# Kernel optimization log

Hardware: AMD Instinct MI355X
Metric: run time of the kernel (lower is better)

## Reference

```python
import jax, jax.numpy as jnp
import numpy as np
from jax import lax

NUM_CLASSES = 80
TOPK = 13
ALPHA = 1.0
BETA = 6.0
EPS = 1e-9
P = 150000
N = 256


def _make_boxes(key, n, scale):
    k1, k2 = jax.random.split(key)
    xy = jax.random.uniform(k1, (n, 2), dtype=jnp.float32) * scale
    wh = jax.random.uniform(k2, (n, 2), dtype=jnp.float32) * (0.2 * scale) + 1.0
    return jnp.concatenate([xy, xy + wh], axis=-1)  # valid x1y1x2y2


def setup_inputs() -> dict:
    key = jax.random.key(0)
    k1, k2, k3, k4 = jax.random.split(key, 4)
    cls_pred = jax.random.uniform(k1, (P, NUM_CLASSES), dtype=jnp.float32)
    bbox_pred = _make_boxes(k2, P, 640.0)
    bbox_gt = _make_boxes(k3, N, 640.0)
    # FG labels are > 0 (code indexes cls_pred[label-1])
    label_gt = jax.random.randint(k4, (N, 1), 1, NUM_CLASSES + 1, dtype=jnp.int32)
    return {"cls_pred": cls_pred, "bbox_pred": bbox_pred, "label_gt": label_gt, "bbox_gt": bbox_gt}


def _ious(bbox1, bbox2, eps=EPS):
    # bbox1: (N,4) gt, bbox2: (P,4) pred -> (N,P)
    b1 = bbox1[:, None, :]
    b2 = bbox2[None, :, :]
    x1y1 = jnp.maximum(b1[..., 0:2], b2[..., 0:2])
    x2y2 = jnp.minimum(b1[..., 2:4], b2[..., 2:4])
    inter = jnp.clip(x2y2 - x1y1, 0.0).prod(-1)
    area1 = jnp.clip(b1[..., 2:4] - b1[..., 0:2], 0.0).prod(-1)
    area2 = jnp.clip(b2[..., 2:4] - b2[..., 0:2], 0.0).prod(-1)
    return inter / (area1 + area2 - inter + eps)


def _metrics_topk(metrics, topk, eps=EPS):
    n, num_priors = metrics.shape
    topk_vals, topk_idxs = lax.top_k(metrics, topk)  # (N,k)
    keep = topk_vals.max(axis=-1, keepdims=True) > eps
    topk_idxs = jnp.where(keep, topk_idxs, 0)
    rows = jnp.arange(n)[:, None]
    counts = jnp.zeros((n, num_priors), jnp.int32).at[rows, topk_idxs].add(1)
    is_in_topk = jnp.where(counts > 1, 0, counts)
    return is_in_topk.astype(metrics.dtype)


def reference(cls_pred, bbox_pred, label_gt, bbox_gt):
    num_priors, num_classes = cls_pred.shape
    n_gt = bbox_gt.shape[0]
    ious = _ious(bbox_gt, bbox_pred)  # (N,P)
    lbl = label_gt.reshape(-1).astype(jnp.int32)  # (N,)
    bbox_cls_scores = jnp.take(cls_pred.T, lbl - 1, axis=0)  # (N,P)
    alignment_metrics = jnp.power(bbox_cls_scores, ALPHA) * jnp.power(ious, BETA)
    mask_positive = _metrics_topk(alignment_metrics, TOPK)  # (N,P) float 0/1
    mask_positive_sum = mask_positive.sum(axis=0)  # (P,)
    # conflict resolution: priors claimed by >1 gt go to the max-iou gt.
    # Applying unconditionally equals the torch data-dependent branch.
    is_max_iou = (jnp.arange(n_gt)[:, None] == ious.argmax(axis=0)[None, :]).astype(ious.dtype)
    mask_positive = jnp.where(mask_positive_sum[None, :] > 1, is_max_iou, mask_positive)
    mask_positive_sum = mask_positive.sum(axis=0)
    assigned_gt_index = mask_positive.argmax(axis=0)  # (P,)
    assigned_labels = lbl[assigned_gt_index]  # (P,)
    assigned_cls = jax.nn.one_hot(assigned_labels - 1, num_classes, dtype=jnp.int32)
    assigned_bboxes = bbox_gt[assigned_gt_index]  # (P,4)
    assigned_labels = jnp.where(mask_positive_sum > 0, assigned_labels, 0)
    return (assigned_gt_index, assigned_labels, assigned_cls, assigned_bboxes)
```

## Files before the change

### kernel.cpp

```cpp
#include <hip/hip_runtime.h>

#define TOPK 13
#define NCLS 80
#define EPSF 1e-9f
#define NSEG 32
#define GPB  8
#define CAP2 832

__global__ __launch_bounds__(256) void sortgt(const int* __restrict__ lbl,
                                              int* __restrict__ gorder, int N) {
    __shared__ int key[256];
    int t = threadIdx.x;
    key[t] = (t < N) ? ((lbl[t] << 8) | t) : 0x7FFFFFFF;
    __syncthreads();
    for (int k = 2; k <= 256; k <<= 1) {
        for (int j = k >> 1; j >= 1; j >>= 1) {
            int ixj = t ^ j;
            if (ixj > t) {
                int a = key[t], b = key[ixj];
                bool up = ((t & k) == 0);
                if (up ? (a > b) : (a < b)) { key[t] = b; key[ixj] = a; }
            }
            __syncthreads();
        }
    }
    if (t < N) gorder[t] = key[t] & 0xFF;
}

__global__ __launch_bounds__(256) void prep(const float4* __restrict__ cls4,
                                            float* __restrict__ clsT,
                                            int* __restrict__ count,
                                            int* __restrict__ firstg, int P) {
    __shared__ float tile[64 * 81];
    int p0 = blockIdx.x * 64;
    int valid = P - p0; if (valid > 64) valid = 64;
    int t = threadIdx.x;
    int limq = valid * 20;
    for (int f = t; f < 64 * 20; f += 256) {
        int pl = f / 20, cq = f - pl * 20;
        float4 v = (f < limq) ? cls4[(size_t)p0 * 20 + f] : make_float4(0, 0, 0, 0);
        tile[pl * 81 + 4 * cq + 0] = v.x;
        tile[pl * 81 + 4 * cq + 1] = v.y;
        tile[pl * 81 + 4 * cq + 2] = v.z;
        tile[pl * 81 + 4 * cq + 3] = v.w;
    }
    if (t < 64 && t < valid) { count[p0 + t] = 0; firstg[p0 + t] = 0x7FFFFFFF; }
    __syncthreads();
    for (int f = t; f < 80 * 16; f += 256) {
        int c = f >> 4, j4 = f & 15;
        int j = 4 * j4;
        if (j < valid) {
            float4 o;
            o.x = tile[(j + 0) * 81 + c];
            o.y = tile[(j + 1) * 81 + c];
            o.z = tile[(j + 2) * 81 + c];
            o.w = tile[(j + 3) * 81 + c];
            *(float4*)&clsT[(size_t)c * P + p0 + j] = o;
        }
    }
}

__global__ __launch_bounds__(512, 4) void phaseA1(const float* __restrict__ clsT,
                                                  const float4* __restrict__ bboxp,
                                                  const float4* __restrict__ bboxg,
                                                  const int* __restrict__ lbl,
                                                  const int* __restrict__ gorder,
                                                  float2* __restrict__ cand,
                                                  int P, int N, int seglen) {
#pragma clang fp contract(off)
    const int s = blockIdx.x, tile = blockIdx.y, t = threadIdx.x;
    const int wv = t >> 6, lane = t & 63;
    const int pstart = s * seglen;
    int pend = pstart + seglen; if (pend > P) pend = P;

    __shared__ float2 buf[GPB][CAP2];
    __shared__ int ctr[GPB];

    float4 gb[GPB]; float ga[GPB]; int coff[GPB];
#pragma unroll
    for (int j = 0; j < GPB; j++) {
        int gi8 = tile * GPB + j;
        int gj = (gi8 < N) ? gorder[gi8] : -1;
        if (gj >= 0) {
            gb[j] = bboxg[gj];
            int c = lbl[gj] - 1;
            coff[j] = c * P;
        } else {
            gb[j] = make_float4(0.0f, 0.0f, 0.0f, 0.0f);
            coff[j] = 0;
        }
        ga[j] = fmaxf(gb[j].z - gb[j].x, 0.0f) * fmaxf(gb[j].w - gb[j].y, 0.0f);
    }
    const bool myValid = (tile * GPB + wv) < N;
    if (t < GPB) ctr[t] = 0;
    __syncthreads();

    bool first = true;
    for (int p = pstart + t; p < pend; p += 512) {
        float4 pb = bboxp[p];
        float pa = fmaxf(pb.z - pb.x, 0.0f) * fmaxf(pb.w - pb.y, 0.0f);
        bool force = first && (t < 16);
        first = false;
        float sc[GPB];
#pragma unroll
        for (int j = 0; j < GPB; j++) sc[j] = clsT[coff[j] + p];
#pragma unroll
        for (int j = 0; j < GPB; j++) {
            float xx1 = fmaxf(gb[j].x, pb.x), yy1 = fmaxf(gb[j].y, pb.y);
            float xx2 = fminf(gb[j].z, pb.z), yy2 = fminf(gb[j].w, pb.w);
            float inter = fmaxf(xx2 - xx1, 0.0f) * fmaxf(yy2 - yy1, 0.0f);
            float iou = inter / (((ga[j] + pa) - inter) + EPSF);
            float i2 = iou * iou;
            float m = sc[j] * ((i2 * i2) * i2);
            bool want = (m > 0.0f) || force;
            if (want) {
                int slot = atomicAdd(&ctr[j], 1);
                if (slot < CAP2) buf[j][slot] = make_float2(m, __int_as_float(p));
            }
        }
    }
    __syncthreads();

    const int total = ctr[wv];
    float v[TOPK]; int id[TOPK];
#pragma unroll
    for (int k = 0; k < TOPK; k++) { v[k] = -1.0f; id[k] = 0x7FFFFFFF; }

    auto ins = [&](float m, int p) {
        bool b12 = (m > v[TOPK - 1]) || (m == v[TOPK - 1] && p < id[TOPK - 1]);
        if (b12) {
#pragma unroll
            for (int k = TOPK - 1; k >= 1; k--) {
                bool a = (m > v[k - 1]) || (m == v[k - 1] && p < id[k - 1]);
                bool b = (m > v[k]) || (m == v[k] && p < id[k]);
                float nv = a ? v[k - 1] : (b ? m : v[k]);
                int   ni = a ? id[k - 1] : (b ? p : id[k]);
                v[k] = nv; id[k] = ni;
            }
            bool a0 = (m > v[0]) || (m == v[0] && p < id[0]);
            if (a0) { v[0] = m; id[0] = p; }
        }
    };

    if (total <= CAP2) {
        for (int e = lane; e < total; e += 64) {
            float2 E = buf[wv][e];
            ins(E.x, __float_as_int(E.y));
        }
    } else if (myValid) {
        int gj = gorder[tile * GPB + wv];
        float4 gbw = bboxg[gj];
        float gaw = fmaxf(gbw.z - gbw.x, 0.0f) * fmaxf(gbw.w - gbw.y, 0.0f);
        const float* crow = clsT + (size_t)(lbl[gj] - 1) * P;
        for (int p = pstart + lane; p < pend; p += 64) {
            float4 pb = bboxp[p];
            float pa = fmaxf(pb.z - pb.x, 0.0f) * fmaxf(pb.w - pb.y, 0.0f);
            float xx1 = fmaxf(gbw.x, pb.x), yy1 = fmaxf(gbw.y, pb.y);
            float xx2 = fminf(gbw.z, pb.z), yy2 = fminf(gbw.w, pb.w);
            float inter = fmaxf(xx2 - xx1, 0.0f) * fmaxf(yy2 - yy1, 0.0f);
            float iou = inter / (((gaw + pa) - inter) + EPSF);
            float i2 = iou * iou;
            float m = crow[p] * ((i2 * i2) * i2);
            ins(m, p);
        }
    }
    __syncthreads();

    float2* wl = buf[wv];
#pragma unroll
    for (int k = 0; k < TOPK; k++)
        wl[lane * TOPK + k] = make_float2(v[k], __int_as_float(id[k]));
    __syncthreads();
    for (int str = 32; str >= 1; str >>= 1) {
        if (lane < str) {
            float2 merged[TOPK];
            int a = 0, b = 0;
            const int ba = lane * TOPK, bb = (lane + str) * TOPK;
#pragma unroll
            for (int k = 0; k < TOPK; k++) {
                float2 fa = wl[ba + a], fb = wl[bb + b];
                int ia = __float_as_int(fa.y), ib = __float_as_int(fb.y);
                bool takeA = (fa.x > fb.x) || (fa.x == fb.x && ia < ib);
                merged[k] = takeA ? fa : fb;
                a += takeA; b += !takeA;
            }
#pragma unroll
            for (int k = 0; k < TOPK; k++) wl[ba + k] = merged[k];
        }
        __syncthreads();
    }
    if (lane < TOPK && myValid) {
        int gj = gorder[tile * GPB + wv];
        cand[((size_t)gj * NSEG + s) * TOPK + lane] = wl[lane];
    }
}

__global__ __launch_bounds__(512) void phaseA2(const float2* __restrict__ cand,
                                               int* __restrict__ count,
                                               int* __restrict__ firstg) {
    const int g = blockIdx.x;
    const int t = threadIdx.x;
    const int M = NSEG * TOPK;
    __shared__ float cv[512];
    __shared__ int   ci[512];
    if (t < M) {
        float2 e = cand[(size_t)g * M + t];
        cv[t] = e.x; ci[t] = __float_as_int(e.y);
    } else {
        cv[t] = -1.0f; ci[t] = 0x7FFFFFFF;
    }
    __syncthreads();
    for (int k = 2; k <= 512; k <<= 1) {
        for (int j = k >> 1; j >= 1; j >>= 1) {
            int ixj = t ^ j;
            if (ixj > t) {
                float va = cv[t], vb = cv[ixj];
                int   ia = ci[t], ib = ci[ixj];
                bool aBeforeB = (va > vb) || (va == vb && ia < ib);
                bool dirFwd = ((t & k) == 0);
                bool doswap = dirFwd ? !aBeforeB : aBeforeB;
                if (doswap) { cv[t] = vb; ci[t] = ib; cv[ixj] = va; ci[ixj] = ia; }
            }
            __syncthreads();
        }
    }
    if (t < TOPK && cv[0] > EPSF) {
        int pi = ci[t];
        atomicAdd(&count[pi], 1);
        atomicMin(&firstg[pi], g);
    }
}

__global__ __launch_bounds__(256) void phaseCF(const float4* __restrict__ bboxp,
                                               const float4* __restrict__ bboxg,
                                               const int* __restrict__ lbl,
                                               const int* __restrict__ count,
                                               const int* __restrict__ firstg,
                                               float* __restrict__ out0,
                                               float* __restrict__ out1,
                                               float4* __restrict__ outcls4,
                                               float4* __restrict__ outbox4, int P, int N) {
#pragma clang fp contract(off)
    __shared__ float4 gbS[256];
    __shared__ int glS[256];
    __shared__ int gil[256];
    __shared__ int clsl[256];
    int t = threadIdx.x;
    if (t < N) { gbS[t] = bboxg[t]; glS[t] = lbl[t]; }
    __syncthreads();
    int p0 = blockIdx.x * 256;
    int nloc = P - p0; if (nloc > 256) nloc = 256;
    if (t < nloc) {
        int p = p0 + t;
        int cnt = count[p];
        int gi = 0, pos = 0;
        if (cnt == 1) { gi = firstg[p]; pos = 1; }
        else if (cnt > 1) {
            float4 pb = bboxp[p];
            float pa = fmaxf(pb.z - pb.x, 0.0f) * fmaxf(pb.w - pb.y, 0.0f);
            float best = -1.0f;
            for (int g = 0; g < N; g++) {
                float4 g4 = gbS[g];
                float gar = fmaxf(g4.z - g4.x, 0.0f) * fmaxf(g4.w - g4.y, 0.0f);
                float xx1 = fmaxf(g4.x, pb.x), yy1 = fmaxf(g4.y, pb.y);
                float xx2 = fminf(g4.z, pb.z), yy2 = fminf(g4.w, pb.w);
                float inter = fmaxf(xx2 - xx1, 0.0f) * fmaxf(yy2 - yy1, 0.0f);
                float iou = inter / (((gar + pa) - inter) + EPSF);
                if (iou > best) { best = iou; gi = g; }
            }
            pos = 1;
        }
        out0[p] = (float)gi;
        out1[p] = pos ? (float)glS[gi] : 0.0f;
        gil[t] = gi;
        clsl[t] = glS[gi] - 1;
        outbox4[p] = gbS[gi];
    }
    __syncthreads();
    for (int f = t; f < nloc * 20; f += 256) {
        int pl = f / 20, q = f - pl * 20;
        int cl = clsl[pl], c0 = q * 4;
        float4 vv = make_float4(c0 == cl ? 1.0f : 0.0f, c0 + 1 == cl ? 1.0f : 0.0f,
                                c0 + 2 == cl ? 1.0f : 0.0f, c0 + 3 == cl ? 1.0f : 0.0f);
        outcls4[(size_t)p0 * 20 + f] = vv;
    }
}

__global__ __launch_bounds__(256) void phaseC1(const float4* __restrict__ bboxp,
                                               const float4* __restrict__ bboxg,
                                               const int* __restrict__ lbl,
                                               const int* __restrict__ count,
                                               const int* __restrict__ firstg,
                                               float* __restrict__ out0,
                                               float* __restrict__ out1, int P, int N) {
#pragma clang fp contract(off)
    __shared__ float4 gbS[256];
    __shared__ int glS[256];
    if (threadIdx.x < (unsigned)N) {
        gbS[threadIdx.x] = bboxg[threadIdx.x];
        glS[threadIdx.x] = lbl[threadIdx.x];
    }
    __syncthreads();
    int p = blockIdx.x * 256 + threadIdx.x;
    if (p >= P) return;
    int cnt = count[p];
    int gi = 0, pos = 0;
    if (cnt == 1) { gi = firstg[p]; pos = 1; }
    else if (cnt > 1) {
        float4 pb = bboxp[p];
        float pa = fmaxf(pb.z - pb.x, 0.0f) * fmaxf(pb.w - pb.y, 0.0f);
        float best = -1.0f;
        for (int g = 0; g < N; g++) {
            float4 g4 = gbS[g];
            float gar = fmaxf(g4.z - g4.x, 0.0f) * fmaxf(g4.w - g4.y, 0.0f);
            float xx1 = fmaxf(g4.x, pb.x), yy1 = fmaxf(g4.y, pb.y);
            float xx2 = fminf(g4.z, pb.z), yy2 = fminf(g4.w, pb.w);
            float inter = fmaxf(xx2 - xx1, 0.0f) * fmaxf(yy2 - yy1, 0.0f);
            float iou = inter / (((gar + pa) - inter) + EPSF);
            if (iou > best) { best = iou; gi = g; }
        }
        pos = 1;
    }
    out0[p] = (float)gi;
    out1[p] = pos ? (float)glS[gi] : 0.0f;
}

__global__ __launch_bounds__(256) void phaseC2(const float4* __restrict__ bboxg,
                                               const int* __restrict__ lbl,
                                               const float* __restrict__ out0,
                                               float* __restrict__ outcls,
                                               float* __restrict__ outbox, int P, int N) {
    __shared__ float gbb[256 * 4];
    __shared__ int glS[256];
    __shared__ int clsl[256];
    __shared__ int gil[256];
    int tid = threadIdx.x;
    if (tid < N) {
        float4 b = bboxg[tid];
        gbb[tid * 4 + 0] = b.x; gbb[tid * 4 + 1] = b.y;
        gbb[tid * 4 + 2] = b.z; gbb[tid * 4 + 3] = b.w;
        glS[tid] = lbl[tid];
    }
    __syncthreads();
    int p0 = blockIdx.x * 256;
    int nloc = P - p0; if (nloc > 256) nloc = 256;
    if (tid < nloc) {
        int gi = (int)out0[p0 + tid];
        gil[tid] = gi;
        clsl[tid] = glS[gi] - 1;
    }
    __syncthreads();
    for (int f = tid; f < nloc * NCLS; f += 256) {
        int pl = f / NCLS;
        int c  = f - pl * NCLS;
        outcls[(size_t)p0 * NCLS + f] = (c == clsl[pl]) ? 1.0f : 0.0f;
    }
    for (int f = tid; f < nloc * 4; f += 256) {
        int pl = f >> 2, k = f & 3;
        outbox[(size_t)p0 * 4 + f] = gbb[gil[pl] * 4 + k];
    }
}

extern "C" void kernel_launch(void* const* d_in, const int* in_sizes, int n_in,
                              void* d_out, int out_size, void* d_ws, size_t ws_size,
                              hipStream_t stream) {
    const float* cls_pred  = (const float*)d_in[0];
    const float* bbox_pred = (const float*)d_in[1];
    const int*   label_gt  = (const int*)d_in[2];
    const float* bbox_gt   = (const float*)d_in[3];
    int P = in_sizes[1] / 4;
    int N = in_sizes[3] / 4;

    float* out    = (float*)d_out;
    float* out0   = out;
    float* out1   = out + (size_t)P;
    float* outcls = out + (size_t)2 * P;
    float* outbox = out + (size_t)82 * P;

    int tb = (P + 63) / 64;
    int pb = (P + 255) / 256;
    int seglen = (P + NSEG - 1) / NSEG;
    int gtiles = (N + GPB - 1) / GPB;
    dim3 gridA1(NSEG, gtiles);
    size_t candBytes = (size_t)N * NSEG * TOPK * sizeof(float2);
    size_t needWs = (size_t)P * 8 + candBytes + (size_t)N * 4 + 64;

    if (ws_size >= needWs) {
        int*    count  = (int*)d_ws;
        int*    firstg = count + P;
        float2* cand   = (float2*)(firstg + P);
        int*    gorder = (int*)((char*)cand + candBytes);

        sortgt<<<1, 256, 0, stream>>>(label_gt, gorder, N);
        prep<<<tb, 256, 0, stream>>>((const float4*)cls_pred, outcls, count, firstg, P);
        phaseA1<<<gridA1, 512, 0, stream>>>(outcls, (const float4*)bbox_pred,
                                            (const float4*)bbox_gt, label_gt, gorder,
                                            cand, P, N, seglen);
        phaseA2<<<N, 512, 0, stream>>>(cand, count, firstg);
        phaseCF<<<pb, 256, 0, stream>>>((const float4*)bbox_pred, (const float4*)bbox_gt,
                                        label_gt, count, firstg, out0, out1,
                                        (float4*)outcls, (float4*)outbox, P, N);
    } else {
        int*    count  = (int*)outbox;
        int*    firstg = ((int*)outbox) + P;
        float2* cand   = (float2*)(((int*)outbox) + 2 * (size_t)P);
        int*    gorder = (int*)((char*)cand + candBytes);

        sortgt<<<1, 256, 0, stream>>>(label_gt, gorder, N);
        prep<<<tb, 256, 0, stream>>>((const float4*)cls_pred, outcls, count, firstg, P);
        phaseA1<<<gridA1, 512, 0, stream>>>(outcls, (const float4*)bbox_pred,
                                            (const float4*)bbox_gt, label_gt, gorder,
                                            cand, P, N, seglen);
        phaseA2<<<N, 512, 0, stream>>>(cand, count, firstg);
        phaseC1<<<pb, 256, 0, stream>>>((const float4*)bbox_pred, (const float4*)bbox_gt,
                                        label_gt, count, firstg, out0, out1, P, N);
        phaseC2<<<pb, 256, 0, stream>>>((const float4*)bbox_gt, label_gt, out0,
                                        outcls, outbox, P, N);
    }
}
```

Measured before the change: 232.9 us.

## Drop class-score transpose; filter priors by box overlap before scoring

Removes the prep kernel that transposed the full class-score matrix into a column layout. The first pass of phaseA1 now only tests geometric overlap and buffers overlapping prior indices per GT. Scores are then gathered directly from the row-major cls_pred for those candidates only. The counters are initialised with memsets instead. This avoids reading and writing the whole 150000x80 matrix, at the cost of strided gathers and a second bbox read per candidate. firstg is memset to 0x7F7F7F7F rather than 0x7FFFFFFF, which may matter if later code relies on the exact sentinel.

```diff
diff --git a/kernel.cpp b/kernel.cpp
--- a/kernel.cpp
+++ b/kernel.cpp
@@ -5,7 +5,8 @@
 #define EPSF 1e-9f
 #define NSEG 32
 #define GPB  8
-#define CAP2 832
+#define CAP3 512
+#define MCAP (64 * TOPK)
 
 __global__ __launch_bounds__(256) void sortgt(const int* __restrict__ lbl,
                                               int* __restrict__ gorder, int N) {
@@ -27,40 +28,7 @@
     if (t < N) gorder[t] = key[t] & 0xFF;
 }
 
-__global__ __launch_bounds__(256) void prep(const float4* __restrict__ cls4,
-                                            float* __restrict__ clsT,
-                                            int* __restrict__ count,
-                                            int* __restrict__ firstg, int P) {
-    __shared__ float tile[64 * 81];
-    int p0 = blockIdx.x * 64;
-    int valid = P - p0; if (valid > 64) valid = 64;
-    int t = threadIdx.x;
-    int limq = valid * 20;
-    for (int f = t; f < 64 * 20; f += 256) {
-        int pl = f / 20, cq = f - pl * 20;
-        float4 v = (f < limq) ? cls4[(size_t)p0 * 20 + f] : make_float4(0, 0, 0, 0);
-        tile[pl * 81 + 4 * cq + 0] = v.x;
-        tile[pl * 81 + 4 * cq + 1] = v.y;
-        tile[pl * 81 + 4 * cq + 2] = v.z;
-        tile[pl * 81 + 4 * cq + 3] = v.w;
-    }
-    if (t < 64 && t < valid) { count[p0 + t] = 0; firstg[p0 + t] = 0x7FFFFFFF; }
-    __syncthreads();
-    for (int f = t; f < 80 * 16; f += 256) {
-        int c = f >> 4, j4 = f & 15;
-        int j = 4 * j4;
-        if (j < valid) {
-            float4 o;
-            o.x = tile[(j + 0) * 81 + c];
-            o.y = tile[(j + 1) * 81 + c];
-            o.z = tile[(j + 2) * 81 + c];
-            o.w = tile[(j + 3) * 81 + c];
-            *(float4*)&clsT[(size_t)c * P + p0 + j] = o;
-        }
-    }
-}
-
-__global__ __launch_bounds__(512, 4) void phaseA1(const float* __restrict__ clsT,
+__global__ __launch_bounds__(512, 4) void phaseA1(const float* __restrict__ cls,
                                                   const float4* __restrict__ bboxp,
                                                   const float4* __restrict__ bboxg,
                                                   const int* __restrict__ lbl,
@@ -73,55 +41,46 @@
     const int pstart = s * seglen;
     int pend = pstart + seglen; if (pend > P) pend = P;
 
-    __shared__ float2 buf[GPB][CAP2];
+    __shared__ int pbuf[GPB][CAP3];
+    __shared__ float2 mbuf[GPB][MCAP];
     __shared__ int ctr[GPB];
 
-    float4 gb[GPB]; float ga[GPB]; int coff[GPB];
+    float4 gb[GPB];
 #pragma unroll
     for (int j = 0; j < GPB; j++) {
         int gi8 = tile * GPB + j;
         int gj = (gi8 < N) ? gorder[gi8] : -1;
-        if (gj >= 0) {
-            gb[j] = bboxg[gj];
-            int c = lbl[gj] - 1;
-            coff[j] = c * P;
-        } else {
-            gb[j] = make_float4(0.0f, 0.0f, 0.0f, 0.0f);
-            coff[j] = 0;
-        }
-        ga[j] = fmaxf(gb[j].z - gb[j].x, 0.0f) * fmaxf(gb[j].w - gb[j].y, 0.0f);
-    }
-    const bool myValid = (tile * GPB + wv) < N;
+        gb[j] = (gj >= 0) ? bboxg[gj] : make_float4(0.f, 0.f, 0.f, 0.f);
+    }
     if (t < GPB) ctr[t] = 0;
     __syncthreads();
 
     bool first = true;
     for (int p = pstart + t; p < pend; p += 512) {
         float4 pb = bboxp[p];
-        float pa = fmaxf(pb.z - pb.x, 0.0f) * fmaxf(pb.w - pb.y, 0.0f);
         bool force = first && (t < 16);
         first = false;
-        float sc[GPB];
-#pragma unroll
-        for (int j = 0; j < GPB; j++) sc[j] = clsT[coff[j] + p];
 #pragma unroll
         for (int j = 0; j < GPB; j++) {
-            float xx1 = fmaxf(gb[j].x, pb.x), yy1 = fmaxf(gb[j].y, pb.y);
-            float xx2 = fminf(gb[j].z, pb.z), yy2 = fminf(gb[j].w, pb.w);
-            float inter = fmaxf(xx2 - xx1, 0.0f) * fmaxf(yy2 - yy1, 0.0f);
-            float iou = inter / (((ga[j] + pa) - inter) + EPSF);
-            float i2 = iou * iou;
-            float m = sc[j] * ((i2 * i2) * i2);
-            bool want = (m > 0.0f) || force;
+            float dx = fminf(gb[j].z, pb.z) - fmaxf(gb[j].x, pb.x);
+            float dy = fminf(gb[j].w, pb.w) - fmaxf(gb[j].y, pb.y);
+            bool want = ((dx > 0.0f) && (dy > 0.0f)) || force;
             if (want) {
                 int slot = atomicAdd(&ctr[j], 1);
-                if (slot < CAP2) buf[j][slot] = make_float2(m, __int_as_float(p));
-            }
-        }
-    }
-    __syncthreads();
-
-    const int total = ctr[wv];
+                if (slot < CAP3) pbuf[j][slot] = p;
+            }
+        }
+    }
+    __syncthreads();
+
+    const int gi8 = tile * GPB + wv;
+    const bool myValid = gi8 < N;
+    const int gj = myValid ? gorder[gi8] : 0;
+    const float4 gbw = bboxg[gj];
+    const float gaw = fmaxf(gbw.z - gbw.x, 0.0f) * fmaxf(gbw.w - gbw.y, 0.0f);
+    const int cidx = lbl[gj] - 1;
+    const int rawtotal = ctr[wv];
+
     float v[TOPK]; int id[TOPK];
 #pragma unroll
     for (int k = 0; k < TOPK; k++) { v[k] = -1.0f; id[k] = 0x7FFFFFFF; }
@@ -142,31 +101,36 @@
         }
     };
 
-    if (total <= CAP2) {
-        for (int e = lane; e < total; e += 64) {
-            float2 E = buf[wv][e];
-            ins(E.x, __float_as_int(E.y));
-        }
-    } else if (myValid) {
-        int gj = gorder[tile * GPB + wv];
-        float4 gbw = bboxg[gj];
-        float gaw = fmaxf(gbw.z - gbw.x, 0.0f) * fmaxf(gbw.w - gbw.y, 0.0f);
-        const float* crow = clsT + (size_t)(lbl[gj] - 1) * P;
-        for (int p = pstart + lane; p < pend; p += 64) {
+    if (rawtotal <= CAP3) {
+        for (int e = lane; e < rawtotal; e += 64) {
+            int p = pbuf[wv][e];
             float4 pb = bboxp[p];
+            float sc = cls[(size_t)p * NCLS + cidx];
             float pa = fmaxf(pb.z - pb.x, 0.0f) * fmaxf(pb.w - pb.y, 0.0f);
             float xx1 = fmaxf(gbw.x, pb.x), yy1 = fmaxf(gbw.y, pb.y);
             float xx2 = fminf(gbw.z, pb.z), yy2 = fminf(gbw.w, pb.w);
             float inter = fmaxf(xx2 - xx1, 0.0f) * fmaxf(yy2 - yy1, 0.0f);
             float iou = inter / (((gaw + pa) - inter) + EPSF);
             float i2 = iou * iou;
-            float m = crow[p] * ((i2 * i2) * i2);
+            float m = sc * ((i2 * i2) * i2);
             ins(m, p);
         }
-    }
-    __syncthreads();
-
-    float2* wl = buf[wv];
+    } else if (myValid) {
+        for (int p = pstart + lane; p < pend; p += 64) {
+            float4 pb = bboxp[p];
+            float sc = cls[(size_t)p * NCLS + cidx];
+            float pa = fmaxf(pb.z - pb.x, 0.0f) * fmaxf(pb.w - pb.y, 0.0f);
+            float xx1 = fmaxf(gbw.x, pb.x), yy1 = fmaxf(gbw.y, pb.y);
+            float xx2 = fminf(gbw.z, pb.z), yy2 = fminf(gbw.w, pb.w);
+            float inter = fmaxf(xx2 - xx1, 0.0f) * fmaxf(yy2 - yy1, 0.0f);
+            float iou = inter / (((gaw + pa) - inter) + EPSF);
+            float i2 = iou * iou;
+            float m = sc * ((i2 * i2) * i2);
+            ins(m, p);
+        }
+    }
+
+    float2* wl = mbuf[wv];
 #pragma unroll
     for (int k = 0; k < TOPK; k++)
         wl[lane * TOPK + k] = make_float2(v[k], __int_as_float(id[k]));
@@ -189,10 +153,8 @@
         }
         __syncthreads();
     }
-    if (lane < TOPK && myValid) {
-        int gj = gorder[tile * GPB + wv];
+    if (lane < TOPK && myValid)
         cand[((size_t)gj * NSEG + s) * TOPK + lane] = wl[lane];
-    }
 }
 
 __global__ __launch_bounds__(512) void phaseA2(const float2* __restrict__ cand,
@@ -377,7 +339,6 @@
     float* outcls = out + (size_t)2 * P;
     float* outbox = out + (size_t)82 * P;
 
-    int tb = (P + 63) / 64;
     int pb = (P + 255) / 256;
     int seglen = (P + NSEG - 1) / NSEG;
     int gtiles = (N + GPB - 1) / GPB;
@@ -391,9 +352,10 @@
         float2* cand   = (float2*)(firstg + P);
         int*    gorder = (int*)((char*)cand + candBytes);
 
+        hipMemsetAsync(count, 0, (size_t)P * sizeof(int), stream);
+        hipMemsetAsync(firstg, 0x7F, (size_t)P * sizeof(int), stream);
         sortgt<<<1, 256, 0, stream>>>(label_gt, gorder, N);
-        prep<<<tb, 256, 0, stream>>>((const float4*)cls_pred, outcls, count, firstg, P);
-        phaseA1<<<gridA1, 512, 0, stream>>>(outcls, (const float4*)bbox_pred,
+        phaseA1<<<gridA1, 512, 0, stream>>>(cls_pred, (const float4*)bbox_pred,
                                             (const float4*)bbox_gt, label_gt, gorder,
                                             cand, P, N, seglen);
         phaseA2<<<N, 512, 0, stream>>>(cand, count, firstg);
@@ -406,9 +368,10 @@
         float2* cand   = (float2*)(((int*)outbox) + 2 * (size_t)P);
         int*    gorder = (int*)((char*)cand + candBytes);
 
+        hipMemsetAsync(count, 0, (size_t)P * sizeof(int), stream);
+        hipMemsetAsync(firstg, 0x7F, (size_t)P * sizeof(int), stream);
         sortgt<<<1, 256, 0, stream>>>(label_gt, gorder, N);
-        prep<<<tb, 256, 0, stream>>>((const float4*)cls_pred, outcls, count, firstg, P);
-        phaseA1<<<gridA1, 512, 0, stream>>>(outcls, (const float4*)bbox_pred,
+        phaseA1<<<gridA1, 512, 0, stream>>>(cls_pred, (const float4*)bbox_pred,
                                             (const float4*)bbox_gt, label_gt, gorder,
                                             cand, P, N, seglen);
         phaseA2<<<N, 512, 0, stream>>>(cand, count, firstg);
```

Measured after the change: 221.5 us. 4.9% less time.
